# Kernel tuning notes

Hardware: AMD Instinct MI355X
Metric: run time of the kernel (lower is better)

The kernel has to match this reference:

```python
import jax, jax.numpy as jnp
import numpy as np

N_NODES = 50000
N_EDGES = 800000
IN_DIM = 128
OUT_DIM = 64


def setup_inputs() -> dict:
    key = jax.random.key(0)
    k_x, k_r, k_c, k_v, k_w = jax.random.split(key, 5)
    x = jax.random.normal(k_x, (N_NODES, IN_DIM), dtype=jnp.float32)
    edge_row = jax.random.randint(k_r, (N_EDGES,), 0, N_NODES, dtype=jnp.int64)
    edge_col = jax.random.randint(k_c, (N_EDGES,), 0, N_NODES, dtype=jnp.int64)
    edge_val = jax.random.uniform(k_v, (N_EDGES,), dtype=jnp.float32)
    # kaiming_uniform-style init: bound = sqrt(6 / fan_in) with a=sqrt(5) gain folded in torch;
    # exact init values don't affect correctness testing, use a uniform of similar scale.
    bound = float(np.sqrt(6.0 / IN_DIM))
    weight = jax.random.uniform(k_w, (IN_DIM, OUT_DIM), dtype=jnp.float32,
                                minval=-bound, maxval=bound)
    return {"x": x, "edge_row": edge_row, "edge_col": edge_col,
            "edge_val": edge_val, "weight": weight}


def reference(x, edge_row, edge_col, edge_val, weight):
    # dropout p=0.0 -> identity (module default)
    support = x @ weight                              # [N, out_dim] dense GEMM
    # spmm(adj, support): out[i] = sum_e adj_val[e] * support[col[e]] for row[e]==i
    messages = edge_val[:, None] * support[edge_col]  # [E, out_dim] gather
    out = jax.ops.segment_sum(messages, edge_row, num_segments=N_NODES)  # scatter-add
    return jax.nn.relu(out)
```

## Files before the change

### kernel.cpp

```cpp
#include <hip/hip_runtime.h>

#define N_NODES 50000
#define N_EDGES 800000
#define IN_DIM 128
#define OUT_DIM 64

#define GROUP_SHIFT 6
#define GROUP_ROWS 64
#define N_GROUPS 782
#define SLAB 1216
#define CHUNK2 2048
#define FILL_BLOCKS 391

typedef _Float16 h2 __attribute__((ext_vector_type(2)));
typedef _Float16 h4 __attribute__((ext_vector_type(4)));
typedef _Float16 h8 __attribute__((ext_vector_type(8)));
typedef float    f4 __attribute__((ext_vector_type(4)));

#define LDK 136

__global__ __launch_bounds__(256) void fused_gemm_fill(const float* __restrict__ x,
                                                       const float* __restrict__ w,
                                                       const int* __restrict__ erow,
                                                       const int* __restrict__ ecol,
                                                       const float* __restrict__ eval,
                                                       _Float16* __restrict__ support,
                                                       int* __restrict__ gcursor,
                                                       int2* __restrict__ bucket) {
    __shared__ char smem[GROUP_ROWS * LDK * 2 + OUT_DIM * LDK * 2];
    const int tid = threadIdx.x;

    if (blockIdx.x < N_GROUPS) {
        _Float16* xb = (_Float16*)smem;
        _Float16* wt = (_Float16*)(smem + GROUP_ROWS * LDK * 2);

        {
            const int n_s = tid >> 2;
            const int kp0 = tid & 3;
            #pragma unroll
            for (int it = 0; it < 16; ++it) {
                int kp = kp0 + (it << 2);
                int k  = kp << 1;
                h2 hv = { (_Float16)w[(size_t)k * OUT_DIM + n_s],
                          (_Float16)w[(size_t)(k + 1) * OUT_DIM + n_s] };
                *(h2*)&wt[n_s * LDK + k] = hv;
            }
        }
        const int rowbase = blockIdx.x * GROUP_ROWS;
        for (int i = tid; i < GROUP_ROWS * (IN_DIM / 4); i += 256) {
            int r  = i >> 5;
            int kq = i & 31;
            int row = rowbase + r;
            float4 v = (row < N_NODES)
                           ? *(const float4*)&x[(size_t)row * IN_DIM + kq * 4]
                           : make_float4(0.f, 0.f, 0.f, 0.f);
            h4 hv = { (_Float16)v.x, (_Float16)v.y, (_Float16)v.z, (_Float16)v.w };
            *(h4*)&xb[r * LDK + kq * 4] = hv;
        }
        __syncthreads();

        const int wave = tid >> 6;
        const int lane = tid & 63;
        const int mrow = lane & 15;
        const int quad = lane >> 4;
        const int m0   = wave * 16;

        f4 acc[4];
        #pragma unroll
        for (int t = 0; t < 4; ++t) acc[t] = (f4){0.f, 0.f, 0.f, 0.f};

        #pragma unroll
        for (int ks = 0; ks < 4; ++ks) {
            int kof = ks * 32 + quad * 8;
            h8 a = *(h8*)&xb[(m0 + mrow) * LDK + kof];
            #pragma unroll
            for (int t = 0; t < 4; ++t) {
                h8 b = *(h8*)&wt[(t * 16 + mrow) * LDK + kof];
                acc[t] = __builtin_amdgcn_mfma_f32_16x16x32_f16(a, b, acc[t], 0, 0, 0);
            }
        }

        #pragma unroll
        for (int t = 0; t < 4; ++t) {
            #pragma unroll
            for (int r = 0; r < 4; ++r) {
                int row = rowbase + m0 + quad * 4 + r;
                if (row < N_NODES)
                    support[(size_t)row * OUT_DIM + t * 16 + mrow] = (_Float16)acc[t][r];
            }
        }
    } else {
        int* lcnt  = (int*)smem;
        int* lbase = lcnt + N_GROUPS;
        for (int i = tid; i < N_GROUPS; i += 256) lcnt[i] = 0;
        __syncthreads();
        const int base = (blockIdx.x - N_GROUPS) * CHUNK2;
        #pragma unroll 4
        for (int i = 0; i < CHUNK2 / 256; ++i) {
            int e = base + tid + i * 256;
            if (e < N_EDGES) atomicAdd(&lcnt[erow[e] >> GROUP_SHIFT], 1);
        }
        __syncthreads();
        for (int i = tid; i < N_GROUPS; i += 256) {
            int c = lcnt[i];
            lbase[i] = c ? atomicAdd(&gcursor[i], c) : 0;
            lcnt[i]  = 0;
        }
        __syncthreads();
        #pragma unroll 4
        for (int i = 0; i < CHUNK2 / 256; ++i) {
            int e = base + tid + i * 256;
            if (e < N_EDGES) {
                int r = erow[e];
                int g = r >> GROUP_SHIFT;
                int p = atomicAdd(&lcnt[g], 1);
                bucket[(size_t)g * SLAB + lbase[g] + p] =
                    make_int2(((r & (GROUP_ROWS - 1)) << 16) | ecol[e],
                              __float_as_int(eval[e]));
            }
        }
    }
}

__global__ __launch_bounds__(1024) void reduce_group(const int* __restrict__ gcursor,
                                                     const int2* __restrict__ bucket,
                                                     const _Float16* __restrict__ support,
                                                     float* __restrict__ out) {
    __shared__ int2 ebuf[SLAB];
    __shared__ int2 ebuf2[SLAB];
    __shared__ int  rcnt[GROUP_ROWS];
    __shared__ int  rstart[GROUP_ROWS + 1];
    __shared__ int  rcur[GROUP_ROWS];
    const int grp = blockIdx.x;
    const int cnt = min(gcursor[grp], SLAB);
    const size_t sb = (size_t)grp * SLAB;
    const int tid = threadIdx.x;

    if (tid < GROUP_ROWS) rcnt[tid] = 0;
    __syncthreads();
    for (int j = tid; j < cnt; j += 1024) {
        int2 cv = bucket[sb + j];
        ebuf[j] = cv;
        atomicAdd(&rcnt[cv.x >> 16], 1);
    }
    __syncthreads();
    if (tid < GROUP_ROWS) {
        int v = rcnt[tid];
        int s = v;
        #pragma unroll
        for (int off = 1; off < 64; off <<= 1) {
            int t = __shfl_up(s, off, 64);
            if (tid >= off) s += t;
        }
        rstart[tid] = s - v;
        rcur[tid]   = s - v;
        if (tid == 63) rstart[64] = s;
    }
    __syncthreads();
    for (int j = tid; j < cnt; j += 1024) {
        int2 cv = ebuf[j];
        int rl = cv.x >> 16;
        int p  = atomicAdd(&rcur[rl], 1);
        ebuf2[p] = cv;
    }
    __syncthreads();

    const int g  = tid & 15;
    const int lr = tid >> 4;
    const int row = grp * GROUP_ROWS + lr;
    const int jb = rstart[lr];
    const int je = rstart[lr + 1];
    float4 acc = make_float4(0.f, 0.f, 0.f, 0.f);
    for (int j = jb; j < je; ++j) {
        int2 cv = ebuf2[j];
        int col = cv.x & 0xFFFF;
        float v = __int_as_float(cv.y);
        h4 sr = *(const h4*)&support[(size_t)col * OUT_DIM + g * 4];
        acc.x += v * (float)sr[0];
        acc.y += v * (float)sr[1];
        acc.z += v * (float)sr[2];
        acc.w += v * (float)sr[3];
    }
    if (row < N_NODES) {
        acc.x = fmaxf(acc.x, 0.f);
        acc.y = fmaxf(acc.y, 0.f);
        acc.z = fmaxf(acc.z, 0.f);
        acc.w = fmaxf(acc.w, 0.f);
        *(float4*)&out[(size_t)row * OUT_DIM + g * 4] = acc;
    }
}

extern "C" void kernel_launch(void* const* d_in, const int* in_sizes, int n_in,
                              void* d_out, int out_size, void* d_ws, size_t ws_size,
                              hipStream_t stream) {
    const float* x    = (const float*)d_in[0];
    const int*   erow = (const int*)  d_in[1];
    const int*   ecol = (const int*)  d_in[2];
    const float* ev   = (const float*)d_in[3];
    const float* w    = (const float*)d_in[4];
    float* out = (float*)d_out;

    char* ws = (char*)d_ws;
    _Float16* support = (_Float16*)ws;
    int*  gcursor = (int*)(ws + 6400000);
    int2* bucket  = (int2*)(ws + 6403200);

    hipMemsetAsync(gcursor, 0, sizeof(int) * N_GROUPS, stream);

    fused_gemm_fill<<<N_GROUPS + FILL_BLOCKS, 256, 0, stream>>>(
        x, w, erow, ecol, ev, support, gcursor, bucket);

    reduce_group<<<N_GROUPS, 1024, 0, stream>>>(gcursor, bucket, support, out);
}
```

Measured before the change: 128.4 us.

## Front-load fewer, larger fill blocks and unroll gather loop with dual accumulators

The edge-bucketing blocks now come first in the fused launch, so they get scheduled early and overlap with the GEMM blocks. Each one handles 8192 edges instead of 2048, which cuts the number of global cursor atomics and block-level setup. The reduce loop processes two edges per iteration with separate accumulators to expose more memory-level parallelism on the gathered support rows. Larger chunks mean fewer fill blocks, so there is less parallelism in the bucketing phase and it may take longer to finish.

```diff
diff --git a/kernel.cpp b/kernel.cpp
--- a/kernel.cpp
+++ b/kernel.cpp
@@ -9,8 +9,8 @@
 #define GROUP_ROWS 64
 #define N_GROUPS 782
 #define SLAB 1216
-#define CHUNK2 2048
-#define FILL_BLOCKS 391
+#define CHUNK 8192
+#define FILL_BLOCKS 98
 
 typedef _Float16 h2 __attribute__((ext_vector_type(2)));
 typedef _Float16 h4 __attribute__((ext_vector_type(4)));
@@ -30,7 +30,7 @@
     __shared__ char smem[GROUP_ROWS * LDK * 2 + OUT_DIM * LDK * 2];
     const int tid = threadIdx.x;
 
-    if (blockIdx.x < N_GROUPS) {
+    if (blockIdx.x >= FILL_BLOCKS) {
         _Float16* xb = (_Float16*)smem;
         _Float16* wt = (_Float16*)(smem + GROUP_ROWS * LDK * 2);
 
@@ -46,7 +46,7 @@
                 *(h2*)&wt[n_s * LDK + k] = hv;
             }
         }
-        const int rowbase = blockIdx.x * GROUP_ROWS;
+        const int rowbase = (blockIdx.x - FILL_BLOCKS) * GROUP_ROWS;
         for (int i = tid; i < GROUP_ROWS * (IN_DIM / 4); i += 256) {
             int r  = i >> 5;
             int kq = i & 31;
@@ -94,9 +94,9 @@
         int* lbase = lcnt + N_GROUPS;
         for (int i = tid; i < N_GROUPS; i += 256) lcnt[i] = 0;
         __syncthreads();
-        const int base = (blockIdx.x - N_GROUPS) * CHUNK2;
+        const int base = blockIdx.x * CHUNK;
         #pragma unroll 4
-        for (int i = 0; i < CHUNK2 / 256; ++i) {
+        for (int i = 0; i < CHUNK / 256; ++i) {
             int e = base + tid + i * 256;
             if (e < N_EDGES) atomicAdd(&lcnt[erow[e] >> GROUP_SHIFT], 1);
         }
@@ -108,7 +108,7 @@
         }
         __syncthreads();
         #pragma unroll 4
-        for (int i = 0; i < CHUNK2 / 256; ++i) {
+        for (int i = 0; i < CHUNK / 256; ++i) {
             int e = base + tid + i * 256;
             if (e < N_EDGES) {
                 int r = erow[e];
@@ -170,23 +170,41 @@
     const int row = grp * GROUP_ROWS + lr;
     const int jb = rstart[lr];
     const int je = rstart[lr + 1];
-    float4 acc = make_float4(0.f, 0.f, 0.f, 0.f);
-    for (int j = jb; j < je; ++j) {
+    float4 acc0 = make_float4(0.f, 0.f, 0.f, 0.f);
+    float4 acc1 = make_float4(0.f, 0.f, 0.f, 0.f);
+    int j = jb;
+    for (; j + 1 < je; j += 2) {
+        int2 cv0 = ebuf2[j];
+        int2 cv1 = ebuf2[j + 1];
+        float v0 = __int_as_float(cv0.y);
+        float v1 = __int_as_float(cv1.y);
+        h4 s0 = *(const h4*)&support[(size_t)(cv0.x & 0xFFFF) * OUT_DIM + g * 4];
+        h4 s1 = *(const h4*)&support[(size_t)(cv1.x & 0xFFFF) * OUT_DIM + g * 4];
+        acc0.x += v0 * (float)s0[0];
+        acc0.y += v0 * (float)s0[1];
+        acc0.z += v0 * (float)s0[2];
+        acc0.w += v0 * (float)s0[3];
+        acc1.x += v1 * (float)s1[0];
+        acc1.y += v1 * (float)s1[1];
+        acc1.z += v1 * (float)s1[2];
+        acc1.w += v1 * (float)s1[3];
+    }
+    if (j < je) {
         int2 cv = ebuf2[j];
-        int col = cv.x & 0xFFFF;
         float v = __int_as_float(cv.y);
-        h4 sr = *(const h4*)&support[(size_t)col * OUT_DIM + g * 4];
-        acc.x += v * (float)sr[0];
-        acc.y += v * (float)sr[1];
-        acc.z += v * (float)sr[2];
-        acc.w += v * (float)sr[3];
+        h4 sr = *(const h4*)&support[(size_t)(cv.x & 0xFFFF) * OUT_DIM + g * 4];
+        acc0.x += v * (float)sr[0];
+        acc0.y += v * (float)sr[1];
+        acc0.z += v * (float)sr[2];
+        acc0.w += v * (float)sr[3];
     }
     if (row < N_NODES) {
-        acc.x = fmaxf(acc.x, 0.f);
-        acc.y = fmaxf(acc.y, 0.f);
-        acc.z = fmaxf(acc.z, 0.f);
-        acc.w = fmaxf(acc.w, 0.f);
-        *(float4*)&out[(size_t)row * OUT_DIM + g * 4] = acc;
+        float4 a;
+        a.x = fmaxf(acc0.x + acc1.x, 0.f);
+        a.y = fmaxf(acc0.y + acc1.y, 0.f);
+        a.z = fmaxf(acc0.z + acc1.z, 0.f);
+        a.w = fmaxf(acc0.w + acc1.w, 0.f);
+        *(float4*)&out[(size_t)row * OUT_DIM + g * 4] = a;
     }
 }
 
@@ -207,7 +225,7 @@
 
     hipMemsetAsync(gcursor, 0, sizeof(int) * N_GROUPS, stream);
 
-    fused_gemm_fill<<<N_GROUPS + FILL_BLOCKS, 256, 0, stream>>>(
+    fused_gemm_fill<<<FILL_BLOCKS + N_GROUPS, 256, 0, stream>>>(
         x, w, erow, ecol, ev, support, gcursor, bucket);
 
     reduce_group<<<N_GROUPS, 1024, 0, stream>>>(gcursor, bucket, support, out);
```

New measurement: 134.6 us. +4.8%, slower.
